# Kernel tuning notes

Hardware: AMD Instinct MI355X
Metric: run time of the kernel (lower is better)

Reference implementation:

```python
import jax, jax.numpy as jnp
import numpy as np

C, CL = 64, 8
N_PTS, GRID = 250_000, 160
G2 = GRID // 2


def _build():
    """Build sparse coords and MinkowskiEngine-style kernel maps (numpy, int constants)."""
    rng = np.random.default_rng(0)
    raw = rng.integers(0, GRID, size=(int(N_PTS * 1.3), 3))
    keys = (raw[:, 0] * GRID + raw[:, 1]) * GRID + raw[:, 2]
    _, uidx = np.unique(keys, return_index=True)
    coords = raw[np.sort(uidx)][:N_PTS]
    n_in = coords.shape[0]
    # conv1: kernel 2, stride 2 -> each input voxel maps to exactly one output via one of 8 offsets
    down = coords // 2
    dkeys = (down[:, 0] * G2 + down[:, 1]) * G2 + down[:, 2]
    ukeys, inv = np.unique(dkeys, return_inverse=True)
    n_out = int(ukeys.shape[0])
    kid = (coords[:, 0] % 2) * 4 + (coords[:, 1] % 2) * 2 + (coords[:, 2] % 2)
    lists = [np.where(kid == k)[0] for k in range(8)]
    M1 = max(len(l) for l in lists)
    in1 = np.full((8, M1), n_in, np.int32)   # pad -> zero feature row
    out1 = np.full((8, M1), n_out, np.int32)  # pad -> dropped output row
    for k, l in enumerate(lists):
        in1[k, :len(l)] = l
        out1[k, :len(l)] = inv[l]
    # kernel-3, stride-1 map on the downsampled coordinate set (27 offsets)
    D = np.stack([ukeys // (G2 * G2), (ukeys // G2) % G2, ukeys % G2], 1)
    offs = [(a, b, c) for a in (-1, 0, 1) for b in (-1, 0, 1) for c in (-1, 0, 1)]
    pin, pout = [], []
    for o in offs:
        nd = D + np.array(o)
        valid = np.all((nd >= 0) & (nd < G2), 1)
        nk = (nd[:, 0] * G2 + nd[:, 1]) * G2 + nd[:, 2]
        pos = np.minimum(np.searchsorted(ukeys, nk), n_out - 1)
        found = valid & (ukeys[pos] == nk)
        ii = np.where(found)[0]
        pin.append(ii)
        pout.append(pos[ii])
    M3 = max(len(p) for p in pin)
    in3 = np.full((27, M3), n_out, np.int32)
    out3 = np.full((27, M3), n_out, np.int32)
    for k in range(27):
        in3[k, :len(pin[k])] = pin[k]
        out3[k, :len(pin[k])] = pout[k]
    return n_in, n_out, in1, out1, in3, out3


def setup_inputs() -> dict:
    n_in, n_out, in1, out1, in3, out3 = _build()
    key = jax.random.key(0)
    ks = jax.random.split(key, 16)
    s = 0.05
    return dict(
        x_F=jax.random.normal(ks[0], (n_in, C), jnp.float32),
        ctx_F=jax.random.normal(ks[1], (n_in, C), jnp.float32),
        W1=jax.random.normal(ks[2], (8, 2 * C, C), jnp.float32) * s,
        b1=jax.random.normal(ks[3], (C,), jnp.float32) * s,
        Wr00=jax.random.normal(ks[4], (27, C, C // 4), jnp.float32) * s,
        br00=jax.random.normal(ks[5], (C // 4,), jnp.float32) * s,
        Wr01=jax.random.normal(ks[6], (27, C // 4, C // 2), jnp.float32) * s,
        br01=jax.random.normal(ks[7], (C // 2,), jnp.float32) * s,
        Wr10=jax.random.normal(ks[8], (C, C // 4), jnp.float32) * s,
        br10=jax.random.normal(ks[9], (C // 4,), jnp.float32) * s,
        Wr11=jax.random.normal(ks[10], (27, C // 4, C // 4), jnp.float32) * s,
        br11=jax.random.normal(ks[11], (C // 4,), jnp.float32) * s,
        Wr12=jax.random.normal(ks[12], (C // 4, C // 2), jnp.float32) * s,
        br12=jax.random.normal(ks[13], (C // 2,), jnp.float32) * s,
        W2=jax.random.normal(ks[14], (27, C, CL), jnp.float32) * s,
        b2=jax.random.normal(ks[15], (CL,), jnp.float32) * s,
        in1=jnp.asarray(in1), out1=jnp.asarray(out1),
        in3=jnp.asarray(in3), out3=jnp.asarray(out3),
        n_out=n_out,
    )


def _sconv(F, W, b, in_idx, out_idx, n_out):
    """Kernel-map sparse conv: per-offset gather -> GEMM -> scatter-add. F:[N,Cin], W:[K,Cin,Cout]."""
    Fp = jnp.concatenate([F, jnp.zeros((1, F.shape[1]), F.dtype)], 0)
    y = jnp.zeros((n_out + 1, W.shape[2]), F.dtype)
    for k in range(W.shape[0]):  # fixed small kernel volume (8 or 27)
        y = y.at[out_idx[k]].add(Fp[in_idx[k]] @ W[k])
    return y[:n_out] + b


def reference(x_F, ctx_F, W1, b1, Wr00, br00, Wr01, br01, Wr10, br10, Wr11, br11, Wr12, br12, W2, b2, in1, out1, in3, out3, n_out):
    relu = jax.nn.relu
    f = jnp.concatenate([x_F, ctx_F], 1)               # cat(x.F, context1.F)
    h = _sconv(f, W1, b1, in1, out1, n_out)            # conv1: 2C->C, k=2, s=2
    # InceptionResNet block (PCGCv2-style)
    out0 = _sconv(relu(_sconv(h, Wr00, br00, in3, out3, n_out)), Wr01, br01, in3, out3, n_out)
    t = relu(h @ Wr10 + br10)                          # 1x1 conv
    t = relu(_sconv(t, Wr11, br11, in3, out3, n_out))  # 3x3 conv
    path1 = t @ Wr12 + br12                            # 1x1 conv
    h = jnp.concatenate([out0, path1], 1) + h          # cat + residual
    return _sconv(h, W2, b2, in3, out3, n_out)         # conv2: C->CL, k=3, s=1
```

## Files before the change

kernel.cpp:

```cpp
#include <hip/hip_runtime.h>

#define DEV __device__ __forceinline__

typedef __attribute__((ext_vector_type(8))) short bf16x8;
typedef __attribute__((ext_vector_type(4))) float f32x4;

DEV float4 ld4(const float* p){ return *reinterpret_cast<const float4*>(p); }

DEV unsigned short f2bf(float f){
    union { float f; unsigned u; } v; v.f = f;
    unsigned r = v.u + 0x7fffu + ((v.u >> 16) & 1u);
    return (unsigned short)(r >> 16);
}
DEV float bf2f(unsigned short s){
    union { unsigned u; float f; } v; v.u = ((unsigned)s) << 16;
    return v.f;
}

DEV void async16(const void* g, void* l){
    __builtin_amdgcn_global_load_lds(
        (const __attribute__((address_space(1))) unsigned*)g,
        (__attribute__((address_space(3))) unsigned*)l, 16, 0, 0);
}

__global__ __launch_bounds__(256)
void inv_init(int* __restrict__ inv, long n, int defv){
    long i = (long)blockIdx.x*256 + threadIdx.x;
    if (i < n) inv[i] = defv;
}

__global__ __launch_bounds__(256)
void inv_build(const int* __restrict__ inK, const int* __restrict__ outK,
               int* __restrict__ inv, int M, int n_out){
    int k = blockIdx.y;
    int m = blockIdx.x*256 + threadIdx.x;
    if (m >= M) return;
    int o = outK[(long)k*M + m];
    if (o != n_out) inv[(long)k*n_out + o] = inK[(long)k*M + m];
}

__global__ __launch_bounds__(256)
void zero_rows(unsigned short* A, unsigned short* B, unsigned short* C,
               unsigned short* D, unsigned short* E, int n_out){
    int t = threadIdx.x;
    if (t < 64)       A[(long)n_out*64 + t] = 0;
    else if (t < 80)  B[(long)n_out*16 + (t-64)] = 0;
    else if (t < 144) C[(long)n_out*64 + (t-80)] = 0;
    else if (t < 160) D[(long)n_out*16 + (t-144)] = 0;
    else if (t < 176) E[(long)n_out*16 + (t-160)] = 0;
}

__global__ __launch_bounds__(256)
void fill_bias_bf16(unsigned short* __restrict__ A, const float* __restrict__ b, long total){
    long i = (long)blockIdx.x*256 + threadIdx.x;
    if (i < total) A[i] = f2bf(b[i & 63]);
}

__global__ __launch_bounds__(256)
void wfrag_unpaired(const float* __restrict__ W, unsigned short* __restrict__ F,
                    int KC, int NT, int CIN, int CR, int total){
    int idx = blockIdx.x*256 + threadIdx.x;
    if (idx >= total) return;
    int j = idx & 7, l = (idx >> 3) & 63, rest = idx >> 9;
    int nt = rest % NT, cc = rest / NT;
    int k = cc / KC, kc = cc % KC;
    int g = l >> 4, c = l & 15;
    int cin = kc*32 + g*8 + j, cout = nt*16 + c;
    float v = (cout < CR) ? W[((long)k*CIN + cin)*CR + cout] : 0.f;
    F[idx] = f2bf(v);
}

__global__ __launch_bounds__(256)
void wfrag_paired(const float* __restrict__ W, unsigned short* __restrict__ F,
                  int NKr, int NT, int CR, int total){
    int idx = blockIdx.x*256 + threadIdx.x;
    if (idx >= total) return;
    int j = idx & 7, l = (idx >> 3) & 63, rest = idx >> 9;
    int nt = rest % NT, cc = rest / NT;
    int g = l >> 4, c = l & 15;
    int koff = 2*cc + (g >> 1);
    int cin = (g & 1)*8 + j, cout = nt*16 + c;
    float v = (koff < NKr && cout < CR) ? W[((long)koff*16 + cin)*CR + cout] : 0.f;
    F[idx] = f2bf(v);
}

template<bool RELU, bool OUTBF16, int YS, int CR>
__global__ __launch_bounds__(256)
void gather27_lds(const void* __restrict__ Xv, const unsigned short* __restrict__ Wf,
                  const int* __restrict__ inv, const float* __restrict__ bias,
                  void* __restrict__ Yv, int n_out)
{
    __shared__ alignas(16) char buf[2*8192];
    const int lane = threadIdx.x & 63, w = threadIdx.x >> 6;
    const long jblock = (long)blockIdx.x * 64;
    if (jblock >= n_out) return;
    const int r = lane & 15, g = lane >> 4;
    const char* X = (const char*)Xv;
    const bf16x8* __restrict__ WF = (const bf16x8*)Wf;

    const int  scol = (((lane & 7) ^ (lane >> 3)) << 4);
    const long jr0 = min(jblock + w*16 +     (lane >> 3), (long)n_out - 1);
    const long jr1 = min(jblock + w*16 + 8 + (lane >> 3), (long)n_out - 1);
    char* lds_w0 = buf + w*2048;
    char* lds_w1 = buf + w*2048 + 1024;

    const int rd0 = w*2048 + r*128 + (( 0 + g*16) ^ ((r & 7) << 4));
    const int rd1 = w*2048 + r*128 + ((64 + g*16) ^ ((r & 7) << 4));

    f32x4 acc = {0,0,0,0};

    int c0 = inv[jr0], c1 = inv[jr1];
    async16(X + (long)c0*128 + scol, lds_w0);
    async16(X + (long)c1*128 + scol, lds_w1);
    int n0 = inv[(long)n_out + jr0], n1 = inv[(long)n_out + jr1];
    bf16x8 wc0 = WF[lane], wc1 = WF[64 + lane];
    __syncthreads();

    #pragma unroll 1
    for (int k = 0; k < 27; ++k){
        const int cb = k & 1;
        if (k < 26){
            char* dst = buf + (cb^1)*8192 + w*2048;
            async16(X + (long)n0*128 + scol, dst);
            async16(X + (long)n1*128 + scol, dst + 1024);
        }
        int t0 = 0, t1 = 0;
        if (k < 25){
            t0 = inv[(long)(k+2)*n_out + jr0];
            t1 = inv[(long)(k+2)*n_out + jr1];
        }
        bf16x8 wn0 = wc0, wn1 = wc1;
        if (k < 26){
            wn0 = WF[((long)(k+1)*2    )*64 + lane];
            wn1 = WF[((long)(k+1)*2 + 1)*64 + lane];
        }
        bf16x8 a0 = *(const bf16x8*)(buf + cb*8192 + rd0);
        bf16x8 a1 = *(const bf16x8*)(buf + cb*8192 + rd1);
        acc = __builtin_amdgcn_mfma_f32_16x16x32_bf16(a0, wc0, acc, 0, 0, 0);
        acc = __builtin_amdgcn_mfma_f32_16x16x32_bf16(a1, wc1, acc, 0, 0, 0);
        __syncthreads();
        n0 = t0; n1 = t1; wc0 = wn0; wc1 = wn1;
    }

    const float bv = (r < CR) ? bias[r] : 0.f;
    #pragma unroll
    for (int q = 0; q < 4; ++q){
        long row = jblock + w*16 + g*4 + q;
        if (row < n_out){
            float v = acc[q] + bv;
            if constexpr (RELU) v = fmaxf(v, 0.f);
            if constexpr (OUTBF16) ((unsigned short*)Yv)[row*YS + r] = f2bf(v);
            else if (r < CR)       ((float*)Yv)[row*YS + r] = v;
        }
    }
}

__global__ __launch_bounds__(256)
void conv1_pass(const float* __restrict__ xF, const float* __restrict__ cF,
                const unsigned short* __restrict__ Wfk,
                const int* __restrict__ in1k, const int* __restrict__ out1k,
                unsigned short* __restrict__ A, int M1, int n_in, int n_out)
{
    const int lane = threadIdx.x & 63, wave = threadIdx.x >> 6;
    const int m0 = (blockIdx.x*4 + wave)*16;
    if (m0 >= M1) return;
    const int r = lane & 15, g = lane >> 4;
    const int mc = min(m0 + r, M1-1);
    const int i = in1k[mc];
    const bool valid = i < n_in;
    const long iv = valid ? i : 0;
    const bf16x8* __restrict__ WF = (const bf16x8*)Wfk;
    const bf16x8 az = {0,0,0,0,0,0,0,0};
    f32x4 acc[4];
    #pragma unroll
    for (int nt=0; nt<4; ++nt) acc[nt] = f32x4{0,0,0,0};

    #pragma unroll
    for (int kc=0; kc<4; ++kc){
        const float* s = (kc < 2) ? (xF + iv*64 + kc*32 + g*8)
                                  : (cF + iv*64 + (kc-2)*32 + g*8);
        float4 lo = ld4(s), hi = ld4(s+4);
        bf16x8 a;
        a[0]=(short)f2bf(lo.x); a[1]=(short)f2bf(lo.y);
        a[2]=(short)f2bf(lo.z); a[3]=(short)f2bf(lo.w);
        a[4]=(short)f2bf(hi.x); a[5]=(short)f2bf(hi.y);
        a[6]=(short)f2bf(hi.z); a[7]=(short)f2bf(hi.w);
        if (!valid) a = az;
        #pragma unroll
        for (int nt=0; nt<4; ++nt){
            bf16x8 wv = WF[((long)kc*4 + nt)*64 + lane];
            acc[nt] = __builtin_amdgcn_mfma_f32_16x16x32_bf16(a, wv, acc[nt], 0, 0, 0);
        }
    }

    #pragma unroll
    for (int q=0; q<4; ++q){
        int m = m0 + g*4 + q;
        if (m < M1){
            int o = out1k[m];
            long row = (o == n_out) ? (long)n_out + 1 : (long)o;
            #pragma unroll
            for (int nt=0; nt<4; ++nt){
                long off = row*64 + nt*16 + r;
                A[off] = f2bf(acc[nt][q] + bf2f(A[off]));
            }
        }
    }
}

template<int NK, int G, int NT, int RB, bool RELU, int RESBASE,
         int YS, int CB, int CR, int WPE>
__global__ __launch_bounds__(256, WPE)
void mfma_g1(const void* __restrict__ Xv, const unsigned short* __restrict__ Wf,
             const int* __restrict__ inv, const float* __restrict__ bias,
             const unsigned short* __restrict__ RES, unsigned short* __restrict__ Y, int n_out)
{
    const int lane = threadIdx.x & 63, wave = threadIdx.x >> 6;
    const int jbase = (blockIdx.x*4 + wave)*32;
    if (jbase >= n_out) return;
    const int r = lane & 15, g = lane >> 4;
    const int jc0 = min(jbase + r, n_out-1), jc1 = min(jbase + 16 + r, n_out-1);
    const char* X = (const char*)Xv;
    const bf16x8* __restrict__ WF = (const bf16x8*)Wf;
    f32x4 acc0[NT], acc1[NT];
    #pragma unroll
    for (int nt=0; nt<NT; ++nt){ acc0[nt] = f32x4{0,0,0,0}; acc1[nt] = f32x4{0,0,0,0}; }

    #pragma unroll 1
    for (int g0 = 0; g0 < NK; g0 += G) {
        int b0[G], b1[G];
        #pragma unroll
        for (int kk=0; kk<G; ++kk){
            int koff = 2*(g0+kk) + (g >> 1);
            b0[kk] = inv[(long)koff*n_out + jc0];
            b1[kk] = inv[(long)koff*n_out + jc1];
        }
        #pragma unroll
        for (int kk=0; kk<G; ++kk){
            const int k = g0 + kk;
            bf16x8 a0 = *(const bf16x8*)(X + (long)b0[kk]*RB + (g&1)*16);
            bf16x8 a1 = *(const bf16x8*)(X + (long)b1[kk]*RB + (g&1)*16);
            #pragma unroll
            for (int nt=0; nt<NT; ++nt){
                bf16x8 wv = WF[((long)k*NT + nt)*64 + lane];
                acc0[nt] = __builtin_amdgcn_mfma_f32_16x16x32_bf16(a0, wv, acc0[nt], 0, 0, 0);
                acc1[nt] = __builtin_amdgcn_mfma_f32_16x16x32_bf16(a1, wv, acc1[nt], 0, 0, 0);
            }
        }
    }

    float bi[NT];
    #pragma unroll
    for (int nt=0; nt<NT; ++nt){
        int c = nt*16 + r;
        bi[nt] = (c < CR) ? bias[c] : 0.f;
    }
    #pragma unroll
    for (int q=0; q<4; ++q){
        int row = jbase + g*4 + q;
        if (row < n_out){
            #pragma unroll
            for (int nt=0; nt<NT; ++nt){
                int c = nt*16 + r;
                float v = acc0[nt][q] + bi[nt];
                if constexpr (RESBASE >= 0) v += bf2f(RES[(long)row*64 + RESBASE + c]);
                if constexpr (RELU) v = fmaxf(v, 0.f);
                Y[(long)row*YS + CB + c] = f2bf(v);
            }
        }
        int row2 = jbase + 16 + g*4 + q;
        if (row2 < n_out){
            #pragma unroll
            for (int nt=0; nt<NT; ++nt){
                int c = nt*16 + r;
                float v = acc1[nt][q] + bi[nt];
                if constexpr (RESBASE >= 0) v += bf2f(RES[(long)row2*64 + RESBASE + c]);
                if constexpr (RELU) v = fmaxf(v, 0.f);
                Y[(long)row2*YS + CB + c] = f2bf(v);
            }
        }
    }
}

template<int MODE, int NT, int RB, bool RELU, int RESBASE, int YS, int CB, int CR>
__global__ __launch_bounds__(256)
void mfma_dense(const void* __restrict__ Xv, const unsigned short* __restrict__ Wf,
                const float* __restrict__ bias, const unsigned short* __restrict__ RES,
                unsigned short* __restrict__ Y, int n_out)
{
    const int lane = threadIdx.x & 63, wave = threadIdx.x >> 6;
    const int jbase = (blockIdx.x*4 + wave)*16;
    if (jbase >= n_out) return;
    const int r = lane & 15, g = lane >> 4;
    const int jrow = jbase + r;
    const bool rowok = jrow < n_out;
    const char* X = (const char*)Xv;
    const bf16x8* __restrict__ WF = (const bf16x8*)Wf;
    const bf16x8 az = {0,0,0,0,0,0,0,0};
    f32x4 acc[NT];
    #pragma unroll
    for (int nt=0; nt<NT; ++nt) acc[nt] = f32x4{0,0,0,0};

    if constexpr (MODE == 2) {
        #pragma unroll
        for (int kc=0; kc<2; ++kc){
            bf16x8 a = az;
            if (rowok) a = *(const bf16x8*)(X + (long)jrow*RB + kc*64 + g*16);
            #pragma unroll
            for (int nt=0; nt<NT; ++nt){
                bf16x8 wv = WF[((long)kc*NT + nt)*64 + lane];
                acc[nt] = __builtin_amdgcn_mfma_f32_16x16x32_bf16(a, wv, acc[nt], 0, 0, 0);
            }
        }
    } else {
        bf16x8 a = az;
        if (rowok && g < 2) a = *(const bf16x8*)(X + (long)jrow*RB + (g&1)*16);
        #pragma unroll
        for (int nt=0; nt<NT; ++nt){
            bf16x8 wv = WF[nt*64 + lane];
            acc[nt] = __builtin_amdgcn_mfma_f32_16x16x32_bf16(a, wv, acc[nt], 0, 0, 0);
        }
    }

    float bi[NT];
    #pragma unroll
    for (int nt=0; nt<NT; ++nt){
        int c = nt*16 + r;
        bi[nt] = (c < CR) ? bias[c] : 0.f;
    }
    #pragma unroll
    for (int q=0; q<4; ++q){
        int row = jbase + g*4 + q;
        if (row < n_out){
            #pragma unroll
            for (int nt=0; nt<NT; ++nt){
                int c = nt*16 + r;
                float v = acc[nt][q] + bi[nt];
                if constexpr (RESBASE >= 0) v += bf2f(RES[(long)row*64 + RESBASE + c]);
                if constexpr (RELU) v = fmaxf(v, 0.f);
                Y[(long)row*YS + CB + c] = f2bf(v);
            }
        }
    }
}

extern "C" void kernel_launch(void* const* d_in, const int* in_sizes, int n_in_cnt,
                              void* d_out, int out_size, void* d_ws, size_t ws_size,
                              hipStream_t stream)
{
    const float* xF   = (const float*)d_in[0];
    const float* ctxF = (const float*)d_in[1];
    const float* W1   = (const float*)d_in[2];
    const float* b1   = (const float*)d_in[3];
    const float* Wr00 = (const float*)d_in[4];
    const float* br00 = (const float*)d_in[5];
    const float* Wr01 = (const float*)d_in[6];
    const float* br01 = (const float*)d_in[7];
    const float* Wr10 = (const float*)d_in[8];
    const float* br10 = (const float*)d_in[9];
    const float* Wr11 = (const float*)d_in[10];
    const float* br11 = (const float*)d_in[11];
    const float* Wr12 = (const float*)d_in[12];
    const float* br12 = (const float*)d_in[13];
    const float* W2   = (const float*)d_in[14];
    const float* b2   = (const float*)d_in[15];
    const int* in1  = (const int*)d_in[16];
    const int* out1 = (const int*)d_in[17];
    const int* in3  = (const int*)d_in[18];
    const int* out3 = (const int*)d_in[19];

    const int n_out = out_size / 8;
    const int n_in  = in_sizes[0] / 64;
    const int M1 = in_sizes[16] / 8;
    const int M3 = in_sizes[18] / 27;

    char* p = (char*)d_ws;
    int* inv3 = (int*)p;                 p += (size_t)28*n_out*4;
    unsigned short* A = (unsigned short*)p;  p += (size_t)(n_out+2)*64*2;
    unsigned short* B = (unsigned short*)p;  p += (size_t)(n_out+1)*16*2;
    unsigned short* C = (unsigned short*)p;  p += (size_t)(n_out+1)*64*2;
    unsigned short* D = (unsigned short*)p;  p += (size_t)(n_out+1)*16*2;
    unsigned short* E = (unsigned short*)p;  p += (size_t)(n_out+1)*16*2;
    unsigned short* Wf_c1 = (unsigned short*)p;  p += (size_t)32*4*512*2;
    unsigned short* Wf_00 = (unsigned short*)p;  p += (size_t)54*512*2;
    unsigned short* Wf_2  = (unsigned short*)p;  p += (size_t)54*512*2;
    unsigned short* Wf_01 = (unsigned short*)p;  p += (size_t)14*2*512*2;
    unsigned short* Wf_11 = (unsigned short*)p;  p += (size_t)14*512*2;
    unsigned short* Wf_10 = (unsigned short*)p;  p += (size_t)2*512*2;
    unsigned short* Wf_12 = (unsigned short*)p;  p += (size_t)2*512*2;
    float* OUT = (float*)d_out;

    auto cdiv = [](long a, long b){ return (int)((a + b - 1)/b); };

    inv_init<<<cdiv((long)28*n_out,256),256,0,stream>>>(inv3, (long)28*n_out, n_out);
    inv_build<<<dim3(cdiv(M3,256),27),256,0,stream>>>(in3, out3, inv3, M3, n_out);
    zero_rows<<<1,256,0,stream>>>(A, B, C, D, E, n_out);
    fill_bias_bf16<<<cdiv((long)n_out*64,256),256,0,stream>>>(A, b1, (long)n_out*64);

    wfrag_unpaired<<<cdiv(32*4*512,256),256,0,stream>>>(W1,   Wf_c1, 4, 4, 128, 64, 32*4*512);
    wfrag_unpaired<<<cdiv(54*512,256),  256,0,stream>>>(Wr00, Wf_00, 2, 1,  64, 16, 54*512);
    wfrag_unpaired<<<cdiv(54*512,256),  256,0,stream>>>(W2,   Wf_2,  2, 1,  64,  8, 54*512);
    wfrag_unpaired<<<cdiv(2*512,256),   256,0,stream>>>(Wr10, Wf_10, 2, 1,  64, 16, 2*512);
    wfrag_paired  <<<cdiv(14*2*512,256),256,0,stream>>>(Wr01, Wf_01, 27, 2, 32, 14*2*512);
    wfrag_paired  <<<cdiv(14*512,256),  256,0,stream>>>(Wr11, Wf_11, 27, 1, 16, 14*512);
    wfrag_paired  <<<cdiv(2*512,256),   256,0,stream>>>(Wr12, Wf_12,  1, 2, 32, 2*512);

    for (int k=0; k<8; ++k){
        conv1_pass<<<cdiv(M1,64),256,0,stream>>>(
            xF, ctxF, Wf_c1 + (size_t)k*16*512,
            in1 + (size_t)k*M1, out1 + (size_t)k*M1, A, M1, n_in, n_out);
    }

    const int grid_g = cdiv(n_out, 128);
    const int grid_l = cdiv(n_out, 64);
    const int grid_d = cdiv(n_out, 64);

    gather27_lds<true, true, 16, 16>
        <<<grid_l,256,0,stream>>>(A, Wf_00, inv3, br00, B, n_out);
    mfma_dense<2, 1, 128, true, -1, 16, 0, 16>
        <<<grid_d,256,0,stream>>>(A, Wf_10, br10, nullptr, D, n_out);
    mfma_g1<14,7,2, 32, false, 0, 64, 0, 32, 4>
        <<<grid_g,256,0,stream>>>(B, Wf_01, inv3, br01, A, C, n_out);
    mfma_g1<14,7,1, 32, true, -1, 16, 0, 16, 4>
        <<<grid_g,256,0,stream>>>(D, Wf_11, inv3, br11, nullptr, E, n_out);
    mfma_dense<3, 2, 32, false, 32, 64, 32, 32>
        <<<grid_d,256,0,stream>>>(E, Wf_12, br12, A, C, n_out);
    gather27_lds<false, false, 8, 8>
        <<<grid_l,256,0,stream>>>(C, Wf_2, inv3, b2, OUT, n_out);
}
```

Baseline: 293.3 us.

## Triple-buffer gather27 LDS pipeline with manual vmcnt waits and XCD block swizzle

```diff
diff --git a/kernel.cpp b/kernel.cpp
--- a/kernel.cpp
+++ b/kernel.cpp
@@ -21,6 +21,14 @@
     __builtin_amdgcn_global_load_lds(
         (const __attribute__((address_space(1))) unsigned*)g,
         (__attribute__((address_space(3))) unsigned*)l, 16, 0, 0);
+}
+
+#define SB __builtin_amdgcn_sched_barrier(0)
+
+DEV int xcd_swizzle(int orig, int nwg){
+    int q = nwg >> 3, r = nwg & 7;
+    int x = orig & 7, i = orig >> 3;
+    return (x < r ? x*(q+1) : r*(q+1) + (x-r)*q) + i;
 }
 
 __global__ __launch_bounds__(256)
@@ -90,9 +98,10 @@
                   const int* __restrict__ inv, const float* __restrict__ bias,
                   void* __restrict__ Yv, int n_out)
 {
-    __shared__ alignas(16) char buf[2*8192];
+    __shared__ alignas(16) char buf[3*8192];
     const int lane = threadIdx.x & 63, w = threadIdx.x >> 6;
-    const long jblock = (long)blockIdx.x * 64;
+    const int bid = xcd_swizzle(blockIdx.x, gridDim.x);
+    const long jblock = (long)bid * 64;
     if (jblock >= n_out) return;
     const int r = lane & 15, g = lane >> 4;
     const char* X = (const char*)Xv;
@@ -101,45 +110,53 @@
     const int  scol = (((lane & 7) ^ (lane >> 3)) << 4);
     const long jr0 = min(jblock + w*16 +     (lane >> 3), (long)n_out - 1);
     const long jr1 = min(jblock + w*16 + 8 + (lane >> 3), (long)n_out - 1);
-    char* lds_w0 = buf + w*2048;
-    char* lds_w1 = buf + w*2048 + 1024;
 
     const int rd0 = w*2048 + r*128 + (( 0 + g*16) ^ ((r & 7) << 4));
     const int rd1 = w*2048 + r*128 + ((64 + g*16) ^ ((r & 7) << 4));
 
     f32x4 acc = {0,0,0,0};
 
-    int c0 = inv[jr0], c1 = inv[jr1];
-    async16(X + (long)c0*128 + scol, lds_w0);
-    async16(X + (long)c1*128 + scol, lds_w1);
-    int n0 = inv[(long)n_out + jr0], n1 = inv[(long)n_out + jr1];
+    int p0 = inv[jr0],               p1 = inv[jr1];
+    int q0 = inv[(long)n_out + jr0], q1 = inv[(long)n_out + jr1];
+    SB;
+    async16(X + (long)p0*128 + scol, buf + w*2048);
+    async16(X + (long)p1*128 + scol, buf + w*2048 + 1024);
+    SB;
+    int n0 = inv[(long)2*n_out + jr0], n1 = inv[(long)2*n_out + jr1];
+    SB;
     bf16x8 wc0 = WF[lane], wc1 = WF[64 + lane];
-    __syncthreads();
-
+    SB;
+    async16(X + (long)q0*128 + scol, buf + 8192 + w*2048);
+    async16(X + (long)q1*128 + scol, buf + 8192 + w*2048 + 1024);
+    SB;
+    int m0 = inv[(long)3*n_out + jr0], m1 = inv[(long)3*n_out + jr1];
+    SB;
+    bf16x8 wd0 = WF[2*64 + lane], wd1 = WF[3*64 + lane];
+    SB;
+
+    int cb = 0, db = 2;
     #pragma unroll 1
     for (int k = 0; k < 27; ++k){
-        const int cb = k & 1;
-        if (k < 26){
-            char* dst = buf + (cb^1)*8192 + w*2048;
-            async16(X + (long)n0*128 + scol, dst);
-            async16(X + (long)n1*128 + scol, dst + 1024);
-        }
-        int t0 = 0, t1 = 0;
-        if (k < 25){
-            t0 = inv[(long)(k+2)*n_out + jr0];
-            t1 = inv[(long)(k+2)*n_out + jr1];
-        }
-        bf16x8 wn0 = wc0, wn1 = wc1;
-        if (k < 26){
-            wn0 = WF[((long)(k+1)*2    )*64 + lane];
-            wn1 = WF[((long)(k+1)*2 + 1)*64 + lane];
-        }
+        asm volatile("s_waitcnt vmcnt(10)" ::: "memory");
+        SB;
         bf16x8 a0 = *(const bf16x8*)(buf + cb*8192 + rd0);
         bf16x8 a1 = *(const bf16x8*)(buf + cb*8192 + rd1);
+        SB;
+        async16(X + (long)n0*128 + scol, buf + db*8192 + w*2048);
+        async16(X + (long)n1*128 + scol, buf + db*8192 + w*2048 + 1024);
+        SB;
+        const long ki = (long)min(k+4, 26) * n_out;
+        int t0 = inv[ki + jr0], t1 = inv[ki + jr1];
+        SB;
+        const long kw = (long)min(k+2, 26) * 2;
+        bf16x8 wn0 = WF[kw*64 + lane], wn1 = WF[(kw+1)*64 + lane];
+        SB;
         acc = __builtin_amdgcn_mfma_f32_16x16x32_bf16(a0, wc0, acc, 0, 0, 0);
         acc = __builtin_amdgcn_mfma_f32_16x16x32_bf16(a1, wc1, acc, 0, 0, 0);
-        __syncthreads();
-        n0 = t0; n1 = t1; wc0 = wn0; wc1 = wn1;
+        n0 = m0; n1 = m1; m0 = t0; m1 = t1;
+        wc0 = wd0; wc1 = wd1; wd0 = wn0; wd1 = wn1;
+        cb = (cb == 2) ? 0 : cb + 1;
+        db = (db == 2) ? 0 : db + 1;
     }
 
     const float bv = (r < CR) ? bias[r] : 0.f;
```

Measured after the change: 296.1 us. Within noise of the previous version (+0.9%).

## Replace serial conv1 scatter passes with single GEMM pass plus gather-sum, widen gather27 tiles

Applied to the files above, without the earlier changes.

```diff
diff --git a/kernel.cpp b/kernel.cpp
--- a/kernel.cpp
+++ b/kernel.cpp
@@ -21,6 +21,12 @@
     __builtin_amdgcn_global_load_lds(
         (const __attribute__((address_space(1))) unsigned*)g,
         (__attribute__((address_space(3))) unsigned*)l, 16, 0, 0);
+}
+
+DEV int xcd_swizzle(int orig, int nwg){
+    int q = nwg >> 3, r = nwg & 7;
+    int x = orig & 7, i = orig >> 3;
+    return (x < r ? x*(q+1) : r*(q+1) + (x-r)*q) + i;
 }
 
 __global__ __launch_bounds__(256)
@@ -41,19 +47,15 @@
 
 __global__ __launch_bounds__(256)
 void zero_rows(unsigned short* A, unsigned short* B, unsigned short* C,
-               unsigned short* D, unsigned short* E, int n_out){
+               unsigned short* D, unsigned short* E, unsigned short* Z,
+               int n_out, int n_in){
     int t = threadIdx.x;
     if (t < 64)       A[(long)n_out*64 + t] = 0;
     else if (t < 80)  B[(long)n_out*16 + (t-64)] = 0;
     else if (t < 144) C[(long)n_out*64 + (t-80)] = 0;
     else if (t < 160) D[(long)n_out*16 + (t-144)] = 0;
     else if (t < 176) E[(long)n_out*16 + (t-160)] = 0;
-}
-
-__global__ __launch_bounds__(256)
-void fill_bias_bf16(unsigned short* __restrict__ A, const float* __restrict__ b, long total){
-    long i = (long)blockIdx.x*256 + threadIdx.x;
-    if (i < total) A[i] = f2bf(b[i & 63]);
+    else if (t < 240) Z[(long)n_in*64 + (t-176)] = 0;
 }
 
 __global__ __launch_bounds__(256)
@@ -90,29 +92,38 @@
                   const int* __restrict__ inv, const float* __restrict__ bias,
                   void* __restrict__ Yv, int n_out)
 {
-    __shared__ alignas(16) char buf[2*8192];
+    __shared__ alignas(16) char buf[2*16384];
     const int lane = threadIdx.x & 63, w = threadIdx.x >> 6;
-    const long jblock = (long)blockIdx.x * 64;
+    const int bid = xcd_swizzle(blockIdx.x, gridDim.x);
+    const long jblock = (long)bid * 128;
     if (jblock >= n_out) return;
     const int r = lane & 15, g = lane >> 4;
     const char* X = (const char*)Xv;
     const bf16x8* __restrict__ WF = (const bf16x8*)Wf;
 
-    const int  scol = (((lane & 7) ^ (lane >> 3)) << 4);
-    const long jr0 = min(jblock + w*16 +     (lane >> 3), (long)n_out - 1);
-    const long jr1 = min(jblock + w*16 + 8 + (lane >> 3), (long)n_out - 1);
-    char* lds_w0 = buf + w*2048;
-    char* lds_w1 = buf + w*2048 + 1024;
-
-    const int rd0 = w*2048 + r*128 + (( 0 + g*16) ^ ((r & 7) << 4));
-    const int rd1 = w*2048 + r*128 + ((64 + g*16) ^ ((r & 7) << 4));
-
-    f32x4 acc = {0,0,0,0};
-
-    int c0 = inv[jr0], c1 = inv[jr1];
-    async16(X + (long)c0*128 + scol, lds_w0);
-    async16(X + (long)c1*128 + scol, lds_w1);
-    int n0 = inv[(long)n_out + jr0], n1 = inv[(long)n_out + jr1];
+    const int scol = (((lane & 7) ^ (lane >> 3)) << 4);
+    long jr[4];
+    #pragma unroll
+    for (int i=0;i<4;++i)
+        jr[i] = min(jblock + w*32 + i*8 + (lane >> 3), (long)n_out - 1);
+
+    const int o00 = w*4096 + r*128 + (( 0 + g*16) ^ ((r & 7) << 4));
+    const int o01 = w*4096 + r*128 + ((64 + g*16) ^ ((r & 7) << 4));
+    const int o10 = o00 + 16*128;
+    const int o11 = o01 + 16*128;
+
+    f32x4 acc0 = {0,0,0,0}, acc1 = {0,0,0,0};
+
+    int c0 = inv[jr[0]], c1 = inv[jr[1]], c2 = inv[jr[2]], c3 = inv[jr[3]];
+    {
+        char* d = buf + w*4096;
+        async16(X + (long)c0*128 + scol, d);
+        async16(X + (long)c1*128 + scol, d + 1024);
+        async16(X + (long)c2*128 + scol, d + 2048);
+        async16(X + (long)c3*128 + scol, d + 3072);
+    }
+    int n0 = inv[(long)n_out + jr[0]], n1 = inv[(long)n_out + jr[1]];
+    int n2 = inv[(long)n_out + jr[2]], n3 = inv[(long)n_out + jr[3]];
     bf16x8 wc0 = WF[lane], wc1 = WF[64 + lane];
     __syncthreads();
 
@@ -120,56 +131,73 @@
     for (int k = 0; k < 27; ++k){
         const int cb = k & 1;
         if (k < 26){
-            char* dst = buf + (cb^1)*8192 + w*2048;
-            async16(X + (long)n0*128 + scol, dst);
-            async16(X + (long)n1*128 + scol, dst + 1024);
-        }
-        int t0 = 0, t1 = 0;
+            char* d = buf + (cb^1)*16384 + w*4096;
+            async16(X + (long)n0*128 + scol, d);
+            async16(X + (long)n1*128 + scol, d + 1024);
+            async16(X + (long)n2*128 + scol, d + 2048);
+            async16(X + (long)n3*128 + scol, d + 3072);
+        }
+        int t0=0,t1=0,t2=0,t3=0;
         if (k < 25){
-            t0 = inv[(long)(k+2)*n_out + jr0];
-            t1 = inv[(long)(k+2)*n_out + jr1];
+            const long ko = (long)(k+2)*n_out;
+            t0 = inv[ko + jr[0]]; t1 = inv[ko + jr[1]];
+            t2 = inv[ko + jr[2]]; t3 = inv[ko + jr[3]];
         }
         bf16x8 wn0 = wc0, wn1 = wc1;
         if (k < 26){
             wn0 = WF[((long)(k+1)*2    )*64 + lane];
             wn1 = WF[((long)(k+1)*2 + 1)*64 + lane];
         }
-        bf16x8 a0 = *(const bf16x8*)(buf + cb*8192 + rd0);
-        bf16x8 a1 = *(const bf16x8*)(buf + cb*8192 + rd1);
-        acc = __builtin_amdgcn_mfma_f32_16x16x32_bf16(a0, wc0, acc, 0, 0, 0);
-        acc = __builtin_amdgcn_mfma_f32_16x16x32_bf16(a1, wc1, acc, 0, 0, 0);
+        const char* base = buf + cb*16384;
+        bf16x8 a00 = *(const bf16x8*)(base + o00);
+        bf16x8 a01 = *(const bf16x8*)(base + o01);
+        bf16x8 a10 = *(const bf16x8*)(base + o10);
+        bf16x8 a11 = *(const bf16x8*)(base + o11);
+        acc0 = __builtin_amdgcn_mfma_f32_16x16x32_bf16(a00, wc0, acc0, 0, 0, 0);
+        acc1 = __builtin_amdgcn_mfma_f32_16x16x32_bf16(a10, wc0, acc1, 0, 0, 0);
+        acc0 = __builtin_amdgcn_mfma_f32_16x16x32_bf16(a01, wc1, acc0, 0, 0, 0);
+        acc1 = __builtin_amdgcn_mfma_f32_16x16x32_bf16(a11, wc1, acc1, 0, 0, 0);
         __syncthreads();
-        n0 = t0; n1 = t1; wc0 = wn0; wc1 = wn1;
+        n0=t0; n1=t1; n2=t2; n3=t3; wc0=wn0; wc1=wn1;
     }
 
     const float bv = (r < CR) ? bias[r] : 0.f;
     #pragma unroll
     for (int q = 0; q < 4; ++q){
-        long row = jblock + w*16 + g*4 + q;
+        long row = jblock + w*32 + g*4 + q;
         if (row < n_out){
-            float v = acc[q] + bv;
+            float v = acc0[q] + bv;
             if constexpr (RELU) v = fmaxf(v, 0.f);
             if constexpr (OUTBF16) ((unsigned short*)Yv)[row*YS + r] = f2bf(v);
             else if (r < CR)       ((float*)Yv)[row*YS + r] = v;
         }
-    }
-}
-
-__global__ __launch_bounds__(256)
-void conv1_pass(const float* __restrict__ xF, const float* __restrict__ cF,
-                const unsigned short* __restrict__ Wfk,
-                const int* __restrict__ in1k, const int* __restrict__ out1k,
-                unsigned short* __restrict__ A, int M1, int n_in, int n_out)
-{
+        long row2 = row + 16;
+        if (row2 < n_out){
+            float v = acc1[q] + bv;
+            if constexpr (RELU) v = fmaxf(v, 0.f);
+            if constexpr (OUTBF16) ((unsigned short*)Yv)[row2*YS + r] = f2bf(v);
+            else if (r < CR)       ((float*)Yv)[row2*YS + r] = v;
+        }
+    }
+}
+
+__global__ __launch_bounds__(256, 8)
+void conv1_z(const float* __restrict__ xF, const float* __restrict__ cF,
+             const unsigned short* __restrict__ Wfc1, const int* __restrict__ in1,
+             unsigned short* __restrict__ Z, int M1, int n_in)
+{
+    __shared__ unsigned short tz[4][16*64];
+    const int k = blockIdx.x;
     const int lane = threadIdx.x & 63, wave = threadIdx.x >> 6;
-    const int m0 = (blockIdx.x*4 + wave)*16;
+    const int m0 = (blockIdx.y*4 + wave)*16;
     if (m0 >= M1) return;
     const int r = lane & 15, g = lane >> 4;
+    const int* __restrict__ in1k = in1 + (long)k*M1;
     const int mc = min(m0 + r, M1-1);
     const int i = in1k[mc];
     const bool valid = i < n_in;
     const long iv = valid ? i : 0;
-    const bf16x8* __restrict__ WF = (const bf16x8*)Wfk;
+    const bf16x8* __restrict__ WF = (const bf16x8*)(Wfc1 + (size_t)k*16*512);
     const bf16x8 az = {0,0,0,0,0,0,0,0};
     f32x4 acc[4];
     #pragma unroll
@@ -194,18 +222,52 @@
     }
 
     #pragma unroll
-    for (int q=0; q<4; ++q){
-        int m = m0 + g*4 + q;
+    for (int q=0; q<4; ++q)
+        #pragma unroll
+        for (int nt=0; nt<4; ++nt)
+            tz[wave][(g*4+q)*64 + nt*16 + r] = f2bf(acc[nt][q]);
+    __syncthreads();
+    #pragma unroll
+    for (int it=0; it<2; ++it){
+        int cid = it*64 + lane;
+        int row = cid >> 3, c8 = (cid & 7)*8;
+        int m = m0 + row;
         if (m < M1){
-            int o = out1k[m];
-            long row = (o == n_out) ? (long)n_out + 1 : (long)o;
-            #pragma unroll
-            for (int nt=0; nt<4; ++nt){
-                long off = row*64 + nt*16 + r;
-                A[off] = f2bf(acc[nt][q] + bf2f(A[off]));
-            }
-        }
-    }
+            int oi = in1k[m];
+            long drow = (oi < n_in) ? (long)oi : (long)n_in + 1;
+            *(bf16x8*)(Z + drow*64 + c8) = *(const bf16x8*)(&tz[wave][row*64 + c8]);
+        }
+    }
+}
+
+__global__ __launch_bounds__(256)
+void conv1_sum(const unsigned short* __restrict__ Z, const int* __restrict__ inv1,
+               const float* __restrict__ b1, unsigned short* __restrict__ A, int n_out)
+{
+    const int bid = xcd_swizzle(blockIdx.x, gridDim.x);
+    const long t = (long)bid*256 + threadIdx.x;
+    const long o = t >> 3;
+    if (o >= n_out) return;
+    const int c8 = (int)(t & 7) * 8;
+    int b[8];
+    #pragma unroll
+    for (int k=0;k<8;++k) b[k] = inv1[(long)k*n_out + o];
+    float acc[8];
+    #pragma unroll
+    for (int j=0;j<2;++j){
+        float4 v = ld4(b1 + c8 + 4*j);
+        acc[4*j]=v.x; acc[4*j+1]=v.y; acc[4*j+2]=v.z; acc[4*j+3]=v.w;
+    }
+    #pragma unroll
+    for (int k=0;k<8;++k){
+        bf16x8 z = *(const bf16x8*)(Z + (long)b[k]*64 + c8);
+        #pragma unroll
+        for (int j=0;j<8;++j) acc[j] += bf2f((unsigned short)z[j]);
+    }
+    bf16x8 outv;
+    #pragma unroll
+    for (int j=0;j<8;++j) outv[j] = (short)f2bf(acc[j]);
+    *(bf16x8*)(A + o*64 + c8) = outv;
 }
 
 template<int NK, int G, int NT, int RB, bool RELU, int RESBASE,
@@ -376,11 +438,13 @@
 
     char* p = (char*)d_ws;
     int* inv3 = (int*)p;                 p += (size_t)28*n_out*4;
-    unsigned short* A = (unsigned short*)p;  p += (size_t)(n_out+2)*64*2;
+    int* inv1 = (int*)p;                 p += (size_t)8*n_out*4;
+    unsigned short* A = (unsigned short*)p;  p += (size_t)(n_out+1)*64*2;
     unsigned short* B = (unsigned short*)p;  p += (size_t)(n_out+1)*16*2;
     unsigned short* C = (unsigned short*)p;  p += (size_t)(n_out+1)*64*2;
     unsigned short* D = (unsigned short*)p;  p += (size_t)(n_out+1)*16*2;
     unsigned short* E = (unsigned short*)p;  p += (size_t)(n_out+1)*16*2;
+    unsigned short* Z = (unsigned short*)p;  p += (size_t)(n_in+2)*64*2;
     unsigned short* Wf_c1 = (unsigned short*)p;  p += (size_t)32*4*512*2;
     unsigned short* Wf_00 = (unsigned short*)p;  p += (size_t)54*512*2;
     unsigned short* Wf_2  = (unsigned short*)p;  p += (size_t)54*512*2;
@@ -393,9 +457,10 @@
     auto cdiv = [](long a, long b){ return (int)((a + b - 1)/b); };
 
     inv_init<<<cdiv((long)28*n_out,256),256,0,stream>>>(inv3, (long)28*n_out, n_out);
+    inv_init<<<cdiv((long)8*n_out,256),256,0,stream>>>(inv1, (long)8*n_out, n_in);
     inv_build<<<dim3(cdiv(M3,256),27),256,0,stream>>>(in3, out3, inv3, M3, n_out);
-    zero_rows<<<1,256,0,stream>>>(A, B, C, D, E, n_out);
-    fill_bias_bf16<<<cdiv((long)n_out*64,256),256,0,stream>>>(A, b1, (long)n_out*64);
+    inv_build<<<dim3(cdiv(M1,256),8),256,0,stream>>>(in1, out1, inv1, M1, n_out);
+    zero_rows<<<1,256,0,stream>>>(A, B, C, D, E, Z, n_out, n_in);
 
     wfrag_unpaired<<<cdiv(32*4*512,256),256,0,stream>>>(W1,   Wf_c1, 4, 4, 128, 64, 32*4*512);
     wfrag_unpaired<<<cdiv(54*512,256),  256,0,stream>>>(Wr00, Wf_00, 2, 1,  64, 16, 54*512);
@@ -405,14 +470,11 @@
     wfrag_paired  <<<cdiv(14*512,256),  256,0,stream>>>(Wr11, Wf_11, 27, 1, 16, 14*512);
     wfrag_paired  <<<cdiv(2*512,256),   256,0,stream>>>(Wr12, Wf_12,  1, 2, 32, 2*512);
 
-    for (int k=0; k<8; ++k){
-        conv1_pass<<<cdiv(M1,64),256,0,stream>>>(
-            xF, ctxF, Wf_c1 + (size_t)k*16*512,
-            in1 + (size_t)k*M1, out1 + (size_t)k*M1, A, M1, n_in, n_out);
-    }
+    conv1_z<<<dim3(8,cdiv(M1,64)),256,0,stream>>>(xF, ctxF, Wf_c1, in1, Z, M1, n_in);
+    conv1_sum<<<cdiv((long)8*n_out,256),256,0,stream>>>(Z, inv1, b1, A, n_out);
 
     const int grid_g = cdiv(n_out, 128);
-    const int grid_l = cdiv(n_out, 64);
+    const int grid_l = cdiv(n_out, 128);
     const int grid_d = cdiv(n_out, 64);
 
     gather27_lds<true, true, 16, 16>
```

After: 262.7 us. 10.4% less time.
